# Kernel tuning notes

Measured on AMD Instinct MI355X. Metric: run time of the kernel, lower is better.

Reference implementation:

```python
import jax, jax.numpy as jnp
import numpy as np

WS = 8          # window size
SHIFT = WS // 2 # cyclic shift for shifted windows
HEADS = 6
C = 192
EMB = 256
HID = 4 * C
EPS = 1e-5


def _inorm(x):
    # InstanceNorm2d (affine=False): normalize each (sample, channel) over spatial dims
    m = x.mean(axis=(2, 3), keepdims=True)
    v = x.var(axis=(2, 3), keepdims=True)
    return (x - m) * jax.lax.rsqrt(v + EPS)


def _rel_index(ws):
    c = jnp.stack(jnp.meshgrid(jnp.arange(ws), jnp.arange(ws), indexing='ij'), -1).reshape(-1, 2)
    r = c[:, None] - c[None, :] + (ws - 1)          # (N,N,2) in [0, 2ws-2]
    return r[..., 0] * (2 * ws - 1) + r[..., 1]     # (N,N)


def _attn_mask(H, W, ws, shift):
    # standard Swin shifted-window mask: tokens from different pre-shift regions can't attend
    def ids(L):
        a = jnp.arange(L)
        return (a >= L - ws).astype(jnp.int32) + (a >= L - shift).astype(jnp.int32)
    img = ids(H)[:, None] * 3 + ids(W)[None, :]                     # (H,W)
    imgw = img.reshape(H // ws, ws, W // ws, ws).transpose(0, 2, 1, 3).reshape(-1, ws * ws)  # (nW,N)
    return jnp.where(imgw[:, None, :] != imgw[:, :, None], -1e9, 0.0)  # (nW,N,N)


def setup_inputs() -> dict:
    key = jax.random.key(0)
    ks = jax.random.split(key, 12)
    s = 0.02
    return {
        'x':        jax.random.normal(ks[0], (8, C, 128, 128), jnp.float32),
        'cond':     jax.random.normal(ks[1], (8, EMB), jnp.float32),
        'qkv_w':    jax.random.normal(ks[2], (3 * C, C), jnp.float32) * s,
        'qkv_b':    jnp.zeros((3 * C,), jnp.float32),
        'proj_w':   jax.random.normal(ks[3], (C, C), jnp.float32) * s,
        'proj_b':   jnp.zeros((C,), jnp.float32),
        'rel_bias': jax.random.normal(ks[4], ((2 * WS - 1) ** 2, HEADS), jnp.float32) * s,
        'film_w':   jax.random.normal(ks[5], (2 * C, EMB), jnp.float32) * s,
        'film_b':   jnp.zeros((2 * C,), jnp.float32),
        'mlp_w1':   jax.random.normal(ks[6], (HID, C), jnp.float32) * s,
        'mlp_b1':   jnp.zeros((HID,), jnp.float32),
        'mlp_w2':   jax.random.normal(ks[7], (C, HID), jnp.float32) * s,
        'mlp_b2':   jnp.zeros((C,), jnp.float32),
    }


def reference(x, cond, qkv_w, qkv_b, proj_w, proj_b, rel_bias,
              film_w, film_b, mlp_w1, mlp_b1, mlp_w2, mlp_b2):
    B, Cc, H, W = x.shape
    N = WS * WS
    nW = (H // WS) * (W // WS)
    hd = Cc // HEADS

    # ---- x = x + attn(norm1(x)) : shifted window attention ----
    xn = _inorm(x)
    xs = jnp.roll(xn, (-SHIFT, -SHIFT), axis=(2, 3))
    # window partition -> (B, nW, N, C)
    xw = (xs.reshape(B, Cc, H // WS, WS, W // WS, WS)
            .transpose(0, 2, 4, 3, 5, 1)
            .reshape(B, nW, N, Cc))
    qkv = xw @ qkv_w.T + qkv_b                       # (B,nW,N,3C)
    q, k, v = jnp.split(qkv, 3, axis=-1)
    def heads(t):
        return t.reshape(B, nW, N, HEADS, hd).transpose(0, 1, 3, 2, 4)  # (B,nW,H,N,hd)
    q, k, v = heads(q), heads(k), heads(v)
    attn = jnp.einsum('bwhnd,bwhmd->bwhnm', q, k) * (hd ** -0.5)
    bias = rel_bias[_rel_index(WS)].transpose(2, 0, 1)   # (HEADS,N,N)
    mask = _attn_mask(H, W, WS, SHIFT)                   # (nW,N,N)
    attn = attn + bias[None, None] + mask[None, :, None]
    a = jax.nn.softmax(attn, axis=-1)
    o = jnp.einsum('bwhnm,bwhmd->bwhnd', a, v)
    o = o.transpose(0, 1, 3, 2, 4).reshape(B, nW, N, Cc)
    o = o @ proj_w.T + proj_b
    # window reverse -> (B,C,H,W), undo shift
    o = (o.reshape(B, H // WS, W // WS, WS, WS, Cc)
           .transpose(0, 5, 1, 3, 2, 4)
           .reshape(B, Cc, H, W))
    o = jnp.roll(o, (SHIFT, SHIFT), axis=(2, 3))
    x = x + o

    # ---- x = x + mlp(FiLM(norm2(x), cond)) ----
    h = _inorm(x)
    gb = cond @ film_w.T + film_b                     # (B,2C)
    scale, shift = gb[:, :Cc], gb[:, Cc:]
    h = h * (1.0 + scale)[:, :, None, None] + shift[:, :, None, None]
    h = jnp.einsum('bchw,oc->bohw', h, mlp_w1) + mlp_b1[None, :, None, None]
    h = jax.nn.gelu(h, approximate=True)              # GELU('tanh')
    h = jnp.einsum('bchw,oc->bohw', h, mlp_w2) + mlp_b2[None, :, None, None]
    return x + h
```

## Files before the change

kernel.cpp:

```cpp
#include <hip/hip_runtime.h>
#include <hip/hip_bf16.h>

using bf16 = __hip_bfloat16;

#define HEADS 6
#define EPSV 1e-5f
#define QS 0.17677669529663687f

typedef __bf16 bfv8 __attribute__((ext_vector_type(8)));
typedef short sv8 __attribute__((ext_vector_type(8)));
typedef float fv4 __attribute__((ext_vector_type(4)));

__device__ __forceinline__ float bf2f(bf16 h) { return __bfloat162float(h); }

__device__ __forceinline__ unsigned short f2bfbits(float f) {
  union { float f; unsigned u; } x{f};
  unsigned r = x.u + 0x7fffu + ((x.u >> 16) & 1u);
  return (unsigned short)(r >> 16);
}

__device__ __forceinline__ int swz(int row, int col, int rowstride) {
  return row * rowstride + ((((col >> 3) ^ (row & 7)) << 3) | (col & 7));
}

__device__ __forceinline__ uint2 pack4b(fv4 a, float b0, float b1, float b2, float b3) {
  uint2 r;
  r.x = (unsigned)f2bfbits(a[0] + b0) | ((unsigned)f2bfbits(a[1] + b1) << 16);
  r.y = (unsigned)f2bfbits(a[2] + b2) | ((unsigned)f2bfbits(a[3] + b3) << 16);
  return r;
}

template <bool BW>
__device__ __forceinline__ bfv8 ldwf(const short* wb, const float* wf, int row,
                                     int k, int ld, float scale) {
  if constexpr (BW) {
    return *(const bfv8*)(wb + (size_t)row * ld + k);
  } else {
    const float* p = wf + (size_t)row * ld + k;
    float4 a = *(const float4*)p;
    float4 b = *(const float4*)(p + 4);
    sv8 s;
    s[0] = (short)f2bfbits(a.x * scale); s[1] = (short)f2bfbits(a.y * scale);
    s[2] = (short)f2bfbits(a.z * scale); s[3] = (short)f2bfbits(a.w * scale);
    s[4] = (short)f2bfbits(b.x * scale); s[5] = (short)f2bfbits(b.y * scale);
    s[6] = (short)f2bfbits(b.z * scale); s[7] = (short)f2bfbits(b.w * scale);
    return __builtin_bit_cast(bfv8, s);
  }
}

__global__ __launch_bounds__(256) void stats_kernel(const float* __restrict__ x,
                                                    float* __restrict__ mean,
                                                    float* __restrict__ rstd) {
  int bc = blockIdx.x;
  const float4* p = (const float4*)(x + (size_t)bc * 16384);
  float s = 0.f, s2 = 0.f;
  for (int i = threadIdx.x; i < 4096; i += 256) {
    float4 v = p[i];
    s += v.x + v.y + v.z + v.w;
    s2 = fmaf(v.x, v.x, s2);
    s2 = fmaf(v.y, v.y, s2);
    s2 = fmaf(v.z, v.z, s2);
    s2 = fmaf(v.w, v.w, s2);
  }
#pragma unroll
  for (int off = 32; off > 0; off >>= 1) {
    s += __shfl_down(s, off);
    s2 += __shfl_down(s2, off);
  }
  __shared__ float rs[4], rs2[4];
  int wid = threadIdx.x >> 6;
  if ((threadIdx.x & 63) == 0) { rs[wid] = s; rs2[wid] = s2; }
  __syncthreads();
  if (threadIdx.x == 0) {
    float S = rs[0] + rs[1] + rs[2] + rs[3];
    float S2 = rs2[0] + rs2[1] + rs2[2] + rs2[3];
    float m = S * (1.f / 16384.f);
    float v = S2 * (1.f / 16384.f) - m * m;
    mean[bc] = m;
    rstd[bc] = rsqrtf(v + EPSV);
  }
}

__device__ __forceinline__ void pack8(float4 a, float4 b, float sc, short* dst) {
  uint4 o;
  o.x = (unsigned)f2bfbits(a.x * sc) | ((unsigned)f2bfbits(a.y * sc) << 16);
  o.y = (unsigned)f2bfbits(a.z * sc) | ((unsigned)f2bfbits(a.w * sc) << 16);
  o.z = (unsigned)f2bfbits(b.x * sc) | ((unsigned)f2bfbits(b.y * sc) << 16);
  o.w = (unsigned)f2bfbits(b.z * sc) | ((unsigned)f2bfbits(b.w * sc) << 16);
  *(uint4*)dst = o;
}

__global__ __launch_bounds__(256) void fc_kernel(
    const float* __restrict__ cond, const float* __restrict__ fw,
    const float* __restrict__ fb, float* __restrict__ gb,
    const float* __restrict__ qkv_w, const float* __restrict__ proj_w,
    const float* __restrict__ mlp_w1, const float* __restrict__ mlp_w2,
    short* __restrict__ wbA, int nUnits) {
  int bid = blockIdx.x;
  if (bid < 12) {
    int g = bid * 256 + threadIdx.x;
    if (g >= 8 * 384) return;
    int b = g / 384, o = g % 384;
    const float* c = cond + b * 256;
    const float* w = fw + o * 256;
    float acc = fb[o];
    for (int k = 0; k < 256; k += 4) {
      float4 cv = *(const float4*)(c + k);
      float4 wv = *(const float4*)(w + k);
      acc = fmaf(cv.x, wv.x, acc);
      acc = fmaf(cv.y, wv.y, acc);
      acc = fmaf(cv.z, wv.z, acc);
      acc = fmaf(cv.w, wv.w, acc);
    }
    gb[g] = acc;
    return;
  }
  int u = (bid - 12) * 256 + threadIdx.x;
  if (u >= nUnits) return;
  if (u < 18432) {
    int e = u * 8;
    float sc = (e < 36864) ? QS : 1.f;
    const float* src = (e < 110592) ? (qkv_w + e) : (proj_w + (e - 110592));
    pack8(*(const float4*)src, *(const float4*)(src + 4), sc, wbA + e);
  } else if (u < 36864) {
    int f = (u - 18432) * 8;
    int ob = f / 12288, s = f % 12288;
    int row = s / 192, within = s % 192;
    int col0 = (((within >> 3) ^ (row & 7)) << 3);
    const float* src = mlp_w1 + (size_t)(ob * 64 + row) * 192 + col0;
    pack8(*(const float4*)src, *(const float4*)(src + 4), 1.f, wbA + 147456 + f);
  } else {
    int f = (u - 36864) * 8;
    int ob = f / 12288, s = f % 12288;
    int row = s / 64, within = s % 64;
    int ol = (((within >> 3) ^ (row & 7)) << 3);
    const float* src = mlp_w2 + (size_t)row * 768 + ob * 64 + ol;
    pack8(*(const float4*)src, *(const float4*)(src + 4), 1.f, wbA + 294912 + f);
  }
}

template <bool BW>
__global__ __launch_bounds__(512, 4) void attn_mfma2_kernel(
    const float* __restrict__ x, const float* __restrict__ mean,
    const float* __restrict__ rstd, const short* __restrict__ wb,
    const float* __restrict__ qkv_w, const float* __restrict__ qkv_b,
    const float* __restrict__ proj_w, const float* __restrict__ proj_b,
    const float* __restrict__ rel_bias, float* __restrict__ out) {
  __shared__ __align__(16) short s_x[64 * 192];
  __shared__ __align__(16) short s_k[64 * 192];
  __shared__ __align__(16) short s_v[192 * 64];
  __shared__ float s_rel[1350];

  const short* wbq = wb;
  const short* wbp = wb + 110592;

  int tid = threadIdx.x;
  int blk = ((blockIdx.x & 7) << 8) + (blockIdx.x >> 3);
  int b = blk >> 8;
  int wdw = blk & 255;
  int wh = wdw >> 4, ww = wdw & 15;
  int lane = tid & 63;
  int w = tid >> 6;
  int nloc = lane & 15, lg = lane >> 4;

  for (int i = tid; i < 1350; i += 512) s_rel[i] = rel_bias[i];

  for (int u = tid; u < 3072; u += 512) {
    int jh = u & 1, ii = (u >> 1) & 7, c = u >> 4;
    int hg = (wh * 8 + ii + 4) & 127;
    int wc0 = (ww * 8 + jh * 4 + 4) & 127;
    float4 v = *(const float4*)&x[((size_t)(b * 192 + c) << 14) + (hg << 7) + wc0];
    float mn = mean[b * 192 + c], rs = rstd[b * 192 + c];
    int n0 = ii * 8 + jh * 4;
    s_x[swz(n0 + 0, c, 192)] = (short)f2bfbits((v.x - mn) * rs);
    s_x[swz(n0 + 1, c, 192)] = (short)f2bfbits((v.y - mn) * rs);
    s_x[swz(n0 + 2, c, 192)] = (short)f2bfbits((v.z - mn) * rs);
    s_x[swz(n0 + 3, c, 192)] = (short)f2bfbits((v.w - mn) * rs);
  }
  __syncthreads();

  for (int half = 0; half < 2; half++) {
    int ptb = half * 2;
    bfv8 xf[2][6];
#pragma unroll
    for (int pp = 0; pp < 2; pp++)
#pragma unroll
      for (int ks = 0; ks < 6; ks++)
        xf[pp][ks] = *(const bfv8*)&s_x[swz((ptb + pp) * 16 + nloc, ks * 32 + lg * 8, 192)];
    __syncthreads();

    for (int t = w; t < 36; t += 8) {
      bool isQK = (t < 24);
      int baserow = isQK ? t * 16 : 384 + (t - 24) * 16;
      float scl = (!BW && t < 12) ? QS : 1.f;
      bfv8 wf[6];
#pragma unroll
      for (int ks = 0; ks < 6; ks++)
        wf[ks] = ldwf<BW>(wbq, qkv_w, baserow + nloc, ks * 32 + lg * 8, 192, scl);
#pragma unroll
      for (int pp = 0; pp < 2; pp++) {
        int pt = ptb + pp;
        fv4 acc = fv4{0.f, 0.f, 0.f, 0.f};
        if (isQK) {
#pragma unroll
          for (int ks = 0; ks < 6; ks++)
            acc = __builtin_amdgcn_mfma_f32_16x16x32_bf16(wf[ks], xf[pp][ks], acc, 0, 0, 0);
          int o0 = t * 16 + lg * 4;
          float4 bb = *(const float4*)&qkv_b[o0];
          float bsc = (t < 12) ? QS : 1.f;
          uint2 pkk = pack4b(acc, bb.x * bsc, bb.y * bsc, bb.z * bsc, bb.w * bsc);
          if (t < 12)
            *(uint2*)&s_x[swz(pt * 16 + nloc, o0, 192)] = pkk;
          else
            *(uint2*)&s_k[swz(pt * 16 + nloc, o0 - 192, 192)] = pkk;
        } else {
#pragma unroll
          for (int ks = 0; ks < 6; ks++)
            acc = __builtin_amdgcn_mfma_f32_16x16x32_bf16(xf[pp][ks], wf[ks], acc, 0, 0, 0);
          int d = (t - 24) * 16 + nloc;
          float bv = qkv_b[384 + d];
          *(uint2*)&s_v[swz(d, pt * 16 + lg * 4, 64)] = pack4b(acc, bv, bv, bv, bv);
        }
      }
    }
  }
  __syncthreads();

  int maskh = (wh == 15), maskw = (ww == 15);
#pragma unroll
  for (int ui = 0; ui < 3; ui++) {
    int u = w * 3 + ui;
    int hh = u >> 2, ng = u & 3;
    int n = ng * 16 + nloc;
    int i1 = n >> 3, j1 = n & 7;
    int gn = (maskh ? (i1 < 4 ? 1 : 2) : 0) * 3 + (maskw ? (j1 < 4 ? 1 : 2) : 0);

    bfv8 qf = *(const bfv8*)&s_x[swz(n, hh * 32 + lg * 8, 192)];
    fv4 sc[4];
#pragma unroll
    for (int mt = 0; mt < 4; mt++) {
      bfv8 kf = *(const bfv8*)&s_k[swz(mt * 16 + nloc, hh * 32 + lg * 8, 192)];
      sc[mt] = __builtin_amdgcn_mfma_f32_16x16x32_bf16(kf, qf, fv4{0.f, 0.f, 0.f, 0.f}, 0, 0, 0);
    }
    float vals[16];
#pragma unroll
    for (int mt = 0; mt < 4; mt++) {
#pragma unroll
      for (int r = 0; r < 4; r++) {
        int m = mt * 16 + lg * 4 + r;
        int i2 = m >> 3, j2 = m & 7;
        int gm = (maskh ? (i2 < 4 ? 1 : 2) : 0) * 3 + (maskw ? (j2 < 4 ? 1 : 2) : 0);
        float v = sc[mt][r] + s_rel[((i1 - i2 + 7) * 15 + (j1 - j2 + 7)) * 6 + hh];
        vals[mt * 4 + r] = (gn == gm) ? v : v - 1e9f;
      }
    }
    float mx = vals[0];
#pragma unroll
    for (int q = 1; q < 16; q++) mx = fmaxf(mx, vals[q]);
    mx = fmaxf(mx, __shfl_xor(mx, 16));
    mx = fmaxf(mx, __shfl_xor(mx, 32));
    float sum = 0.f;
#pragma unroll
    for (int q = 0; q < 16; q++) {
      vals[q] = __expf(vals[q] - mx);
      sum += vals[q];
    }
    sum += __shfl_xor(sum, 16);
    sum += __shfl_xor(sum, 32);
    float inv = 1.f / sum;

    unsigned pk[4][2];
#pragma unroll
    for (int mt = 0; mt < 4; mt++) {
      pk[mt][0] = (unsigned)f2bfbits(vals[mt * 4] * inv) |
                  ((unsigned)f2bfbits(vals[mt * 4 + 1] * inv) << 16);
      pk[mt][1] = (unsigned)f2bfbits(vals[mt * 4 + 2] * inv) |
                  ((unsigned)f2bfbits(vals[mt * 4 + 3] * inv) << 16);
    }
    int sel = lg >> 1;
    int S0 = nloc + ((lg & 1) << 5);
    int S1 = S0 + 16;
    bfv8 pf[2];
#pragma unroll
    for (int ks = 0; ks < 2; ks++) {
      unsigned a0 = (unsigned)__shfl((int)pk[2 * ks][0], S0);
      unsigned b0 = (unsigned)__shfl((int)pk[2 * ks + 1][0], S0);
      unsigned a1 = (unsigned)__shfl((int)pk[2 * ks][1], S0);
      unsigned b1 = (unsigned)__shfl((int)pk[2 * ks + 1][1], S0);
      unsigned a2 = (unsigned)__shfl((int)pk[2 * ks][0], S1);
      unsigned b2 = (unsigned)__shfl((int)pk[2 * ks + 1][0], S1);
      unsigned a3 = (unsigned)__shfl((int)pk[2 * ks][1], S1);
      unsigned b3 = (unsigned)__shfl((int)pk[2 * ks + 1][1], S1);
      uint4 uu;
      uu.x = sel ? b0 : a0;
      uu.y = sel ? b1 : a1;
      uu.z = sel ? b2 : a2;
      uu.w = sel ? b3 : a3;
      pf[ks] = __builtin_bit_cast(bfv8, uu);
    }
#pragma unroll
    for (int dt = 0; dt < 2; dt++) {
      fv4 oa = fv4{0.f, 0.f, 0.f, 0.f};
#pragma unroll
      for (int ks = 0; ks < 2; ks++) {
        bfv8 vf = *(const bfv8*)&s_v[swz(hh * 32 + dt * 16 + nloc, ks * 32 + lg * 8, 64)];
        oa = __builtin_amdgcn_mfma_f32_16x16x32_bf16(vf, pf[ks], oa, 0, 0, 0);
      }
      int d0 = hh * 32 + dt * 16 + lg * 4;
      *(uint2*)&s_x[swz(n, d0, 192)] = pack4b(oa, 0.f, 0.f, 0.f, 0.f);
    }
  }
  __syncthreads();

  {
    int a2 = w >> 1, half = w & 1;
#pragma unroll
    for (int ci = 0; ci < 3; ci++) {
      int ct = a2 * 3 + ci;
      bfv8 wf[6];
#pragma unroll
      for (int ks = 0; ks < 6; ks++)
        wf[ks] = ldwf<BW>(wbp, proj_w, ct * 16 + nloc, ks * 32 + lg * 8, 192, 1.f);
#pragma unroll
      for (int ni = 0; ni < 2; ni++) {
        int nt = half * 2 + ni;
        fv4 acc = fv4{0.f, 0.f, 0.f, 0.f};
#pragma unroll
        for (int ks = 0; ks < 6; ks++) {
          bfv8 of = *(const bfv8*)&s_x[swz(nt * 16 + nloc, ks * 32 + lg * 8, 192)];
          acc = __builtin_amdgcn_mfma_f32_16x16x32_bf16(wf[ks], of, acc, 0, 0, 0);
        }
        int n = nt * 16 + nloc;
        int ii = n >> 3, jj = n & 7;
        int hg = (wh * 8 + ii + 4) & 127;
        int wc = (ww * 8 + jj + 4) & 127;
        float4 pb4 = *(const float4*)&proj_b[ct * 16 + lg * 4];
        const float* pbp = &pb4.x;
#pragma unroll
        for (int r = 0; r < 4; r++) {
          int c = ct * 16 + lg * 4 + r;
          size_t gi = ((size_t)(b * 192 + c) << 14) + (hg << 7) + wc;
          out[gi] = x[gi] + acc[r] + pbp[r];
        }
      }
    }
  }
}

__global__ __launch_bounds__(512, 4) void mlp_mfma2_kernel(
    float* __restrict__ xio, const float* __restrict__ mean,
    const float* __restrict__ rstd, const float* __restrict__ gb,
    const short* __restrict__ w1s, const short* __restrict__ w2s,
    const float* __restrict__ b1, const float* __restrict__ b2) {
  __shared__ __align__(16) short s_pool[128 * 192];
  __shared__ __align__(16) short s_h[128 * 64];
  __shared__ float s_b1[768];
  __shared__ float s_mean[192], s_rstd[192], s_scale[192], s_shift[192], s_b2[192];

  int tid = threadIdx.x;
  int blk = blockIdx.x;
  int b = blk >> 7;
  int p0 = (blk & 127) << 7;
  int lane = tid & 63;
  int w = tid >> 6;

  for (int i = tid; i < 768; i += 512) s_b1[i] = b1[i];
  for (int i = tid; i < 192; i += 512) {
    int bc = b * 192 + i;
    s_mean[i] = mean[bc];
    s_rstd[i] = rstd[bc];
    s_scale[i] = 1.f + gb[b * 384 + i];
    s_shift[i] = gb[b * 384 + 192 + i];
    s_b2[i] = b2[i];
  }
  __syncthreads();

  for (int e = tid; e < 3072; e += 512) {
    int p = e & 127, cb = e >> 7;
    int c0 = cb * 8;
    sv8 pk;
#pragma unroll
    for (int j = 0; j < 8; j++) {
      int c = c0 + j;
      float xv = xio[((size_t)(b * 192 + c) << 14) + p0 + p];
      float hn = (xv - s_mean[c]) * s_rstd[c];
      pk[j] = (short)f2bfbits(hn * s_scale[c] + s_shift[c]);
    }
    *(sv8*)&s_pool[swz(p, c0, 192)] = pk;
  }
  __syncthreads();

  int prow = w * 16 + (lane & 15);
  bfv8 afr[6];
#pragma unroll
  for (int ks = 0; ks < 6; ks++) {
    int c = ks * 32 + (lane >> 4) * 8;
    afr[ks] = *(const bfv8*)&s_pool[swz(prow, c, 192)];
  }

  short* s_w1 = s_pool;
  short* s_w2 = s_pool + 12288;
  char* poolBytes = (char*)s_pool;

  fv4 acc2[12];
#pragma unroll
  for (int i = 0; i < 12; i++) acc2[i] = fv4{0.f, 0.f, 0.f, 0.f};

  for (int ob = 0; ob < 12; ob++) {
    __syncthreads();
    const char* g1 = (const char*)(w1s + ob * 12288);
    const char* g2 = (const char*)(w2s + ob * 12288);
#pragma unroll
    for (int i = 0; i < 3; i++) {
      int ch = w * 3 + i;
      __builtin_amdgcn_global_load_lds(
          (const __attribute__((address_space(1))) void*)(g1 + ch * 1024 + lane * 16),
          (__attribute__((address_space(3))) void*)(poolBytes + ch * 1024), 16, 0, 0);
      __builtin_amdgcn_global_load_lds(
          (const __attribute__((address_space(1))) void*)(g2 + ch * 1024 + lane * 16),
          (__attribute__((address_space(3))) void*)(poolBytes + 24576 + ch * 1024), 16, 0, 0);
    }
    __syncthreads();

#pragma unroll
    for (int it = 0; it < 4; it++) {
      fv4 a1 = fv4{0.f, 0.f, 0.f, 0.f};
      int orow = it * 16 + (lane & 15);
#pragma unroll
      for (int ks = 0; ks < 6; ks++) {
        int c = ks * 32 + (lane >> 4) * 8;
        bfv8 wf = *(const bfv8*)&s_w1[swz(orow, c, 192)];
        a1 = __builtin_amdgcn_mfma_f32_16x16x32_bf16(wf, afr[ks], a1, 0, 0, 0);
      }
      int o0 = ob * 64 + it * 16 + (lane >> 4) * 4;
      unsigned short hb[4];
#pragma unroll
      for (int r = 0; r < 4; r++) {
        float v = a1[r] + s_b1[o0 + r];
        float g = v / (1.f + __expf(-1.5957691216f * fmaf(0.044715f * v * v, v, v)));
        hb[r] = f2bfbits(g);
      }
      uint2 pk;
      pk.x = (unsigned)hb[0] | ((unsigned)hb[1] << 16);
      pk.y = (unsigned)hb[2] | ((unsigned)hb[3] << 16);
      int ol = it * 16 + (lane >> 4) * 4;
      *(uint2*)&s_h[swz(prow, ol, 64)] = pk;
    }

#pragma unroll
    for (int ks2 = 0; ks2 < 2; ks2++) {
      int ol = ks2 * 32 + (lane >> 4) * 8;
      bfv8 hf = *(const bfv8*)&s_h[swz(prow, ol, 64)];
#pragma unroll
      for (int it2 = 0; it2 < 12; it2++) {
        int crow = it2 * 16 + (lane & 15);
        bfv8 w2f = *(const bfv8*)&s_w2[swz(crow, ol, 64)];
        acc2[it2] = __builtin_amdgcn_mfma_f32_16x16x32_bf16(w2f, hf, acc2[it2], 0, 0, 0);
      }
    }
  }

  int p = p0 + w * 16 + (lane & 15);
#pragma unroll
  for (int it2 = 0; it2 < 12; it2++) {
    int c0 = it2 * 16 + (lane >> 4) * 4;
#pragma unroll
    for (int r = 0; r < 4; r++) {
      int c = c0 + r;
      size_t gi = ((size_t)(b * 192 + c) << 14) + p;
      xio[gi] += acc2[it2][r] + s_b2[c];
    }
  }
}

__global__ __launch_bounds__(512, 2) void mlp_mfma_kernel(
    float* __restrict__ xio, const float* __restrict__ mean,
    const float* __restrict__ rstd, const float* __restrict__ gb,
    const float* __restrict__ w1, const float* __restrict__ b1,
    const float* __restrict__ w2, const float* __restrict__ b2) {
  __shared__ __align__(16) short s_a[128 * 192];
  __shared__ __align__(16) short s_h[128 * 64];
  __shared__ __align__(16) short s_w1[64 * 192];
  __shared__ __align__(16) short s_w2[192 * 64];
  __shared__ float s_b1[768];
  __shared__ float s_mean[192], s_rstd[192], s_scale[192], s_shift[192], s_b2[192];

  int tid = threadIdx.x;
  int blk = blockIdx.x;
  int b = blk >> 7;
  int p0 = (blk & 127) << 7;
  int lane = tid & 63;
  int w = tid >> 6;

  for (int i = tid; i < 768; i += 512) s_b1[i] = b1[i];
  for (int i = tid; i < 192; i += 512) {
    int bc = b * 192 + i;
    s_mean[i] = mean[bc];
    s_rstd[i] = rstd[bc];
    s_scale[i] = 1.f + gb[b * 384 + i];
    s_shift[i] = gb[b * 384 + 192 + i];
    s_b2[i] = b2[i];
  }
  __syncthreads();

  for (int e = tid; e < 3072; e += 512) {
    int p = e & 127, cb = e >> 7;
    int c0 = cb * 8;
    sv8 pk;
#pragma unroll
    for (int j = 0; j < 8; j++) {
      int c = c0 + j;
      float xv = xio[((size_t)(b * 192 + c) << 14) + p0 + p];
      float hn = (xv - s_mean[c]) * s_rstd[c];
      pk[j] = (short)f2bfbits(hn * s_scale[c] + s_shift[c]);
    }
    *(sv8*)&s_a[swz(p, c0, 192)] = pk;
  }
  __syncthreads();

  int prow = w * 16 + (lane & 15);
  bfv8 afr[6];
#pragma unroll
  for (int ks = 0; ks < 6; ks++) {
    int c = ks * 32 + (lane >> 4) * 8;
    afr[ks] = *(const bfv8*)&s_a[swz(prow, c, 192)];
  }

  fv4 acc2[12];
#pragma unroll
  for (int i = 0; i < 12; i++) acc2[i] = fv4{0.f, 0.f, 0.f, 0.f};

  for (int ob = 0; ob < 12; ob++) {
    __syncthreads();
    for (int e = tid; e < 3072; e += 512) {
      int row = e / 48, ch4 = e % 48;
      float4 v = *(const float4*)&w1[(size_t)(ob * 64 + row) * 192 + ch4 * 4];
      uint2 pk;
      pk.x = (unsigned)f2bfbits(v.x) | ((unsigned)f2bfbits(v.y) << 16);
      pk.y = (unsigned)f2bfbits(v.z) | ((unsigned)f2bfbits(v.w) << 16);
      *(uint2*)&s_w1[swz(row, ch4 * 4, 192)] = pk;
    }
    for (int e = tid; e < 3072; e += 512) {
      int row = e >> 4, o4 = (e & 15) * 4;
      float4 v = *(const float4*)&w2[(size_t)row * 768 + ob * 64 + o4];
      uint2 pk;
      pk.x = (unsigned)f2bfbits(v.x) | ((unsigned)f2bfbits(v.y) << 16);
      pk.y = (unsigned)f2bfbits(v.z) | ((unsigned)f2bfbits(v.w) << 16);
      *(uint2*)&s_w2[swz(row, o4, 64)] = pk;
    }
    __syncthreads();

#pragma unroll
    for (int it = 0; it < 4; it++) {
      fv4 a1 = fv4{0.f, 0.f, 0.f, 0.f};
      int orow = it * 16 + (lane & 15);
#pragma unroll
      for (int ks = 0; ks < 6; ks++) {
        int c = ks * 32 + (lane >> 4) * 8;
        bfv8 wf = *(const bfv8*)&s_w1[swz(orow, c, 192)];
        a1 = __builtin_amdgcn_mfma_f32_16x16x32_bf16(wf, afr[ks], a1, 0, 0, 0);
      }
      int o0 = ob * 64 + it * 16 + (lane >> 4) * 4;
      unsigned short hb[4];
#pragma unroll
      for (int r = 0; r < 4; r++) {
        float v = a1[r] + s_b1[o0 + r];
        float g = v / (1.f + __expf(-1.5957691216f * fmaf(0.044715f * v * v, v, v)));
        hb[r] = f2bfbits(g);
      }
      uint2 pk;
      pk.x = (unsigned)hb[0] | ((unsigned)hb[1] << 16);
      pk.y = (unsigned)hb[2] | ((unsigned)hb[3] << 16);
      int ol = it * 16 + (lane >> 4) * 4;
      *(uint2*)&s_h[swz(prow, ol, 64)] = pk;
    }

#pragma unroll
    for (int ks2 = 0; ks2 < 2; ks2++) {
      int ol = ks2 * 32 + (lane >> 4) * 8;
      bfv8 hf = *(const bfv8*)&s_h[swz(prow, ol, 64)];
#pragma unroll
      for (int it2 = 0; it2 < 12; it2++) {
        int crow = it2 * 16 + (lane & 15);
        bfv8 w2f = *(const bfv8*)&s_w2[swz(crow, ol, 64)];
        acc2[it2] = __builtin_amdgcn_mfma_f32_16x16x32_bf16(w2f, hf, acc2[it2], 0, 0, 0);
      }
    }
  }

  int p = p0 + w * 16 + (lane & 15);
#pragma unroll
  for (int it2 = 0; it2 < 12; it2++) {
    int c0 = it2 * 16 + (lane >> 4) * 4;
#pragma unroll
    for (int r = 0; r < 4; r++) {
      int c = c0 + r;
      size_t gi = ((size_t)(b * 192 + c) << 14) + p;
      xio[gi] += acc2[it2][r] + s_b2[c];
    }
  }
}

extern "C" void kernel_launch(void* const* d_in, const int* in_sizes, int n_in,
                              void* d_out, int out_size, void* d_ws, size_t ws_size,
                              hipStream_t stream) {
  const float* x = (const float*)d_in[0];
  const float* cond = (const float*)d_in[1];
  const float* qkv_w = (const float*)d_in[2];
  const float* qkv_b = (const float*)d_in[3];
  const float* proj_w = (const float*)d_in[4];
  const float* proj_b = (const float*)d_in[5];
  const float* rel_bias = (const float*)d_in[6];
  const float* film_w = (const float*)d_in[7];
  const float* film_b = (const float*)d_in[8];
  const float* mlp_w1 = (const float*)d_in[9];
  const float* mlp_b1 = (const float*)d_in[10];
  const float* mlp_w2 = (const float*)d_in[11];
  const float* mlp_b2 = (const float*)d_in[12];

  float* out = (float*)d_out;
  float* ws = (float*)d_ws;
  float* mean1 = ws;
  float* rstd1 = ws + 1536;
  float* mean2 = ws + 3072;
  float* rstd2 = ws + 4608;
  float* gb = ws + 6144;
  short* wbA = (short*)(ws + 9216);

  bool haveA = ws_size >= (size_t)(36864 + 294912);
  bool haveM = ws_size >= (size_t)(36864 + 3 * 294912);

  int nUnits = haveM ? 55296 : (haveA ? 18432 : 0);
  fc_kernel<<<12 + (nUnits + 255) / 256, 256, 0, stream>>>(
      cond, film_w, film_b, gb, qkv_w, proj_w, mlp_w1, mlp_w2, wbA, nUnits);
  stats_kernel<<<1536, 256, 0, stream>>>(x, mean1, rstd1);

  if (haveA)
    attn_mfma2_kernel<true><<<2048, 512, 0, stream>>>(
        x, mean1, rstd1, wbA, qkv_w, qkv_b, proj_w, proj_b, rel_bias, out);
  else
    attn_mfma2_kernel<false><<<2048, 512, 0, stream>>>(
        x, mean1, rstd1, wbA, qkv_w, qkv_b, proj_w, proj_b, rel_bias, out);

  stats_kernel<<<1536, 256, 0, stream>>>(out, mean2, rstd2);

  if (haveM)
    mlp_mfma2_kernel<<<1024, 512, 0, stream>>>(out, mean2, rstd2, gb,
                                               wbA + 147456, wbA + 294912,
                                               mlp_b1, mlp_b2);
  else
    mlp_mfma_kernel<<<1024, 512, 0, stream>>>(out, mean2, rstd2, gb, mlp_w1,
                                              mlp_b1, mlp_w2, mlp_b2);
}
```

Baseline: 396.4 us.

## Fuse second norm stats into attention epilogue and merge pre-kernels

Computes per-channel partial sums and sums of squares of the attention output inside the attention kernel's projection epilogue, writes them per window block, and reduces them with a small kernel. This replaces the second full read of the output just to compute instance-norm statistics. It also folds the first stats pass into the weight-packing kernel to save a launch, software-pipelines weight loads in the QKV and projection loops, hoists the Q/K/V fragment loads, prefetches residual x values, and vectorises the MLP input staging with float4 loads. The cost is extra registers and workspace, and E[x^2]-m^2 computed from partials may differ slightly in precision.

```diff
diff --git a/kernel.cpp b/kernel.cpp
--- a/kernel.cpp
+++ b/kernel.cpp
@@ -10,8 +10,6 @@
 typedef __bf16 bfv8 __attribute__((ext_vector_type(8)));
 typedef short sv8 __attribute__((ext_vector_type(8)));
 typedef float fv4 __attribute__((ext_vector_type(4)));
-
-__device__ __forceinline__ float bf2f(bf16 h) { return __bfloat162float(h); }
 
 __device__ __forceinline__ unsigned short f2bfbits(float f) {
   union { float f; unsigned u; } x{f};
@@ -48,13 +46,11 @@
   }
 }
 
-__global__ __launch_bounds__(256) void stats_kernel(const float* __restrict__ x,
-                                                    float* __restrict__ mean,
-                                                    float* __restrict__ rstd) {
-  int bc = blockIdx.x;
+__device__ __forceinline__ void stats_body(const float* __restrict__ x, int bc,
+                                           float2* __restrict__ mr, int tid) {
   const float4* p = (const float4*)(x + (size_t)bc * 16384);
   float s = 0.f, s2 = 0.f;
-  for (int i = threadIdx.x; i < 4096; i += 256) {
+  for (int i = tid; i < 4096; i += 256) {
     float4 v = p[i];
     s += v.x + v.y + v.z + v.w;
     s2 = fmaf(v.x, v.x, s2);
@@ -68,17 +64,21 @@
     s2 += __shfl_down(s2, off);
   }
   __shared__ float rs[4], rs2[4];
-  int wid = threadIdx.x >> 6;
-  if ((threadIdx.x & 63) == 0) { rs[wid] = s; rs2[wid] = s2; }
+  int wid = tid >> 6;
+  if ((tid & 63) == 0) { rs[wid] = s; rs2[wid] = s2; }
   __syncthreads();
-  if (threadIdx.x == 0) {
+  if (tid == 0) {
     float S = rs[0] + rs[1] + rs[2] + rs[3];
     float S2 = rs2[0] + rs2[1] + rs2[2] + rs2[3];
     float m = S * (1.f / 16384.f);
     float v = S2 * (1.f / 16384.f) - m * m;
-    mean[bc] = m;
-    rstd[bc] = rsqrtf(v + EPSV);
-  }
+    mr[bc] = make_float2(m, rsqrtf(v + EPSV));
+  }
+}
+
+__global__ __launch_bounds__(256) void stats_kernel(const float* __restrict__ x,
+                                                    float2* __restrict__ mr) {
+  stats_body(x, blockIdx.x, mr, threadIdx.x);
 }
 
 __device__ __forceinline__ void pack8(float4 a, float4 b, float sc, short* dst) {
@@ -90,13 +90,19 @@
   *(uint4*)dst = o;
 }
 
-__global__ __launch_bounds__(256) void fc_kernel(
+__global__ __launch_bounds__(256) void fused_pre_kernel(
+    const float* __restrict__ x, float2* __restrict__ mr1,
     const float* __restrict__ cond, const float* __restrict__ fw,
     const float* __restrict__ fb, float* __restrict__ gb,
     const float* __restrict__ qkv_w, const float* __restrict__ proj_w,
     const float* __restrict__ mlp_w1, const float* __restrict__ mlp_w2,
     short* __restrict__ wbA, int nUnits) {
   int bid = blockIdx.x;
+  if (bid < 1536) {
+    stats_body(x, bid, mr1, threadIdx.x);
+    return;
+  }
+  bid -= 1536;
   if (bid < 12) {
     int g = bid * 256 + threadIdx.x;
     if (g >= 8 * 384) return;
@@ -139,13 +145,36 @@
   }
 }
 
+__global__ __launch_bounds__(64) void reduce2_kernel(const float2* __restrict__ part,
+                                                     float2* __restrict__ mr2) {
+  int bc = blockIdx.x;
+  int b = bc / 192, c = bc % 192;
+  const float2* p = part + (size_t)(b * 256) * 192 + c;
+  float s = 0.f, q = 0.f;
+  for (int k = threadIdx.x; k < 256; k += 64) {
+    float2 v = p[(size_t)k * 192];
+    s += v.x;
+    q += v.y;
+  }
+#pragma unroll
+  for (int off = 32; off > 0; off >>= 1) {
+    s += __shfl_down(s, off);
+    q += __shfl_down(q, off);
+  }
+  if (threadIdx.x == 0) {
+    float m = s * (1.f / 16384.f);
+    float v = q * (1.f / 16384.f) - m * m;
+    mr2[bc] = make_float2(m, rsqrtf(v + EPSV));
+  }
+}
+
 template <bool BW>
-__global__ __launch_bounds__(512, 4) void attn_mfma2_kernel(
-    const float* __restrict__ x, const float* __restrict__ mean,
-    const float* __restrict__ rstd, const short* __restrict__ wb,
-    const float* __restrict__ qkv_w, const float* __restrict__ qkv_b,
-    const float* __restrict__ proj_w, const float* __restrict__ proj_b,
-    const float* __restrict__ rel_bias, float* __restrict__ out) {
+__global__ __launch_bounds__(512, 4) void attn_mfma3_kernel(
+    const float* __restrict__ x, const float2* __restrict__ mr1,
+    const short* __restrict__ wb, const float* __restrict__ qkv_w,
+    const float* __restrict__ qkv_b, const float* __restrict__ proj_w,
+    const float* __restrict__ proj_b, const float* __restrict__ rel_bias,
+    float* __restrict__ out, float2* __restrict__ part) {
   __shared__ __align__(16) short s_x[64 * 192];
   __shared__ __align__(16) short s_k[64 * 192];
   __shared__ __align__(16) short s_v[192 * 64];
@@ -170,12 +199,12 @@
     int hg = (wh * 8 + ii + 4) & 127;
     int wc0 = (ww * 8 + jh * 4 + 4) & 127;
     float4 v = *(const float4*)&x[((size_t)(b * 192 + c) << 14) + (hg << 7) + wc0];
-    float mn = mean[b * 192 + c], rs = rstd[b * 192 + c];
+    float2 mrv = mr1[b * 192 + c];
     int n0 = ii * 8 + jh * 4;
-    s_x[swz(n0 + 0, c, 192)] = (short)f2bfbits((v.x - mn) * rs);
-    s_x[swz(n0 + 1, c, 192)] = (short)f2bfbits((v.y - mn) * rs);
-    s_x[swz(n0 + 2, c, 192)] = (short)f2bfbits((v.z - mn) * rs);
-    s_x[swz(n0 + 3, c, 192)] = (short)f2bfbits((v.w - mn) * rs);
+    s_x[swz(n0 + 0, c, 192)] = (short)f2bfbits((v.x - mrv.x) * mrv.y);
+    s_x[swz(n0 + 1, c, 192)] = (short)f2bfbits((v.y - mrv.x) * mrv.y);
+    s_x[swz(n0 + 2, c, 192)] = (short)f2bfbits((v.z - mrv.x) * mrv.y);
+    s_x[swz(n0 + 3, c, 192)] = (short)f2bfbits((v.w - mrv.x) * mrv.y);
   }
   __syncthreads();
 
@@ -189,14 +218,26 @@
         xf[pp][ks] = *(const bfv8*)&s_x[swz((ptb + pp) * 16 + nloc, ks * 32 + lg * 8, 192)];
     __syncthreads();
 
-    for (int t = w; t < 36; t += 8) {
+    bfv8 wf[6];
+    {
+      int t0 = w;
+      int baserow0 = (t0 < 24) ? t0 * 16 : 384 + (t0 - 24) * 16;
+      float scl0 = (!BW && t0 < 12) ? QS : 1.f;
+#pragma unroll
+      for (int ks = 0; ks < 6; ks++)
+        wf[ks] = ldwf<BW>(wbq, qkv_w, baserow0 + nloc, ks * 32 + lg * 8, 192, scl0);
+    }
+    for (int t = w; t < 36;) {
+      int tn = t + 8;
+      bfv8 wfn[6];
+      if (tn < 36) {
+        int baserown = (tn < 24) ? tn * 16 : 384 + (tn - 24) * 16;
+        float scln = (!BW && tn < 12) ? QS : 1.f;
+#pragma unroll
+        for (int ks = 0; ks < 6; ks++)
+          wfn[ks] = ldwf<BW>(wbq, qkv_w, baserown + nloc, ks * 32 + lg * 8, 192, scln);
+      }
       bool isQK = (t < 24);
-      int baserow = isQK ? t * 16 : 384 + (t - 24) * 16;
-      float scl = (!BW && t < 12) ? QS : 1.f;
-      bfv8 wf[6];
-#pragma unroll
-      for (int ks = 0; ks < 6; ks++)
-        wf[ks] = ldwf<BW>(wbq, qkv_w, baserow + nloc, ks * 32 + lg * 8, 192, scl);
 #pragma unroll
       for (int pp = 0; pp < 2; pp++) {
         int pt = ptb + pp;
@@ -222,11 +263,27 @@
           *(uint2*)&s_v[swz(d, pt * 16 + lg * 4, 64)] = pack4b(acc, bv, bv, bv, bv);
         }
       }
+      if (tn >= 36) break;
+#pragma unroll
+      for (int ks = 0; ks < 6; ks++) wf[ks] = wfn[ks];
+      t = tn;
     }
   }
   __syncthreads();
 
   int maskh = (wh == 15), maskw = (ww == 15);
+  bfv8 qfh[3];
+  bfv8 kfh[3][4];
+#pragma unroll
+  for (int ui = 0; ui < 3; ui++) {
+    int u = w * 3 + ui;
+    int hh = u >> 2, ng = u & 3;
+    int n = ng * 16 + nloc;
+    qfh[ui] = *(const bfv8*)&s_x[swz(n, hh * 32 + lg * 8, 192)];
+#pragma unroll
+    for (int mt = 0; mt < 4; mt++)
+      kfh[ui][mt] = *(const bfv8*)&s_k[swz(mt * 16 + nloc, hh * 32 + lg * 8, 192)];
+  }
 #pragma unroll
   for (int ui = 0; ui < 3; ui++) {
     int u = w * 3 + ui;
@@ -235,13 +292,18 @@
     int i1 = n >> 3, j1 = n & 7;
     int gn = (maskh ? (i1 < 4 ? 1 : 2) : 0) * 3 + (maskw ? (j1 < 4 ? 1 : 2) : 0);
 
-    bfv8 qf = *(const bfv8*)&s_x[swz(n, hh * 32 + lg * 8, 192)];
     fv4 sc[4];
 #pragma unroll
-    for (int mt = 0; mt < 4; mt++) {
-      bfv8 kf = *(const bfv8*)&s_k[swz(mt * 16 + nloc, hh * 32 + lg * 8, 192)];
-      sc[mt] = __builtin_amdgcn_mfma_f32_16x16x32_bf16(kf, qf, fv4{0.f, 0.f, 0.f, 0.f}, 0, 0, 0);
-    }
+    for (int mt = 0; mt < 4; mt++)
+      sc[mt] = __builtin_amdgcn_mfma_f32_16x16x32_bf16(kfh[ui][mt], qfh[ui],
+                                                       fv4{0.f, 0.f, 0.f, 0.f}, 0, 0, 0);
+    bfv8 vfh[2][2];
+#pragma unroll
+    for (int dt = 0; dt < 2; dt++)
+#pragma unroll
+      for (int ks = 0; ks < 2; ks++)
+        vfh[dt][ks] = *(const bfv8*)&s_v[swz(hh * 32 + dt * 16 + nloc, ks * 32 + lg * 8, 64)];
+
     float vals[16];
 #pragma unroll
     for (int mt = 0; mt < 4; mt++) {
@@ -302,10 +364,8 @@
     for (int dt = 0; dt < 2; dt++) {
       fv4 oa = fv4{0.f, 0.f, 0.f, 0.f};
 #pragma unroll
-      for (int ks = 0; ks < 2; ks++) {
-        bfv8 vf = *(const bfv8*)&s_v[swz(hh * 32 + dt * 16 + nloc, ks * 32 + lg * 8, 64)];
-        oa = __builtin_amdgcn_mfma_f32_16x16x32_bf16(vf, pf[ks], oa, 0, 0, 0);
-      }
+      for (int ks = 0; ks < 2; ks++)
+        oa = __builtin_amdgcn_mfma_f32_16x16x32_bf16(vfh[dt][ks], pf[ks], oa, 0, 0, 0);
       int d0 = hh * 32 + dt * 16 + lg * 4;
       *(uint2*)&s_x[swz(n, d0, 192)] = pack4b(oa, 0.f, 0.f, 0.f, 0.f);
     }
@@ -314,13 +374,49 @@
 
   {
     int a2 = w >> 1, half = w & 1;
+    int hgv[2], wcv[2];
+#pragma unroll
+    for (int ni = 0; ni < 2; ni++) {
+      int n = (half * 2 + ni) * 16 + nloc;
+      hgv[ni] = (wh * 8 + (n >> 3) + 4) & 127;
+      wcv[ni] = (ww * 8 + (n & 7) + 4) & 127;
+    }
+    float xres[3][2][4];
 #pragma unroll
     for (int ci = 0; ci < 3; ci++) {
       int ct = a2 * 3 + ci;
-      bfv8 wf[6];
-#pragma unroll
-      for (int ks = 0; ks < 6; ks++)
-        wf[ks] = ldwf<BW>(wbp, proj_w, ct * 16 + nloc, ks * 32 + lg * 8, 192, 1.f);
+#pragma unroll
+      for (int ni = 0; ni < 2; ni++)
+#pragma unroll
+        for (int r = 0; r < 4; r++) {
+          int c = ct * 16 + lg * 4 + r;
+          xres[ci][ni][r] =
+              x[((size_t)(b * 192 + c) << 14) + (hgv[ni] << 7) + wcv[ni]];
+        }
+    }
+
+    float ssum[3][4], ssq[3][4];
+#pragma unroll
+    for (int ci = 0; ci < 3; ci++)
+#pragma unroll
+      for (int r = 0; r < 4; r++) { ssum[ci][r] = 0.f; ssq[ci][r] = 0.f; }
+
+    bfv8 wfp[6];
+#pragma unroll
+    for (int ks = 0; ks < 6; ks++)
+      wfp[ks] = ldwf<BW>(wbp, proj_w, (a2 * 3) * 16 + nloc, ks * 32 + lg * 8, 192, 1.f);
+
+#pragma unroll
+    for (int ci = 0; ci < 3; ci++) {
+      int ct = a2 * 3 + ci;
+      bfv8 wfn[6];
+      if (ci < 2) {
+#pragma unroll
+        for (int ks = 0; ks < 6; ks++)
+          wfn[ks] = ldwf<BW>(wbp, proj_w, (ct + 1) * 16 + nloc, ks * 32 + lg * 8, 192, 1.f);
+      }
+      float4 pb4 = *(const float4*)&proj_b[ct * 16 + lg * 4];
+      const float* pbp = &pb4.x;
 #pragma unroll
       for (int ni = 0; ni < 2; ni++) {
         int nt = half * 2 + ni;
@@ -328,30 +424,60 @@
 #pragma unroll
         for (int ks = 0; ks < 6; ks++) {
           bfv8 of = *(const bfv8*)&s_x[swz(nt * 16 + nloc, ks * 32 + lg * 8, 192)];
-          acc = __builtin_amdgcn_mfma_f32_16x16x32_bf16(wf[ks], of, acc, 0, 0, 0);
+          acc = __builtin_amdgcn_mfma_f32_16x16x32_bf16(wfp[ks], of, acc, 0, 0, 0);
         }
-        int n = nt * 16 + nloc;
-        int ii = n >> 3, jj = n & 7;
-        int hg = (wh * 8 + ii + 4) & 127;
-        int wc = (ww * 8 + jj + 4) & 127;
-        float4 pb4 = *(const float4*)&proj_b[ct * 16 + lg * 4];
-        const float* pbp = &pb4.x;
 #pragma unroll
         for (int r = 0; r < 4; r++) {
           int c = ct * 16 + lg * 4 + r;
-          size_t gi = ((size_t)(b * 192 + c) << 14) + (hg << 7) + wc;
-          out[gi] = x[gi] + acc[r] + pbp[r];
+          size_t gi = ((size_t)(b * 192 + c) << 14) + (hgv[ni] << 7) + wcv[ni];
+          float v = xres[ci][ni][r] + acc[r] + pbp[r];
+          out[gi] = v;
+          ssum[ci][r] += v;
+          ssq[ci][r] = fmaf(v, v, ssq[ci][r]);
         }
       }
-    }
-  }
-}
-
-__global__ __launch_bounds__(512, 4) void mlp_mfma2_kernel(
-    float* __restrict__ xio, const float* __restrict__ mean,
-    const float* __restrict__ rstd, const float* __restrict__ gb,
-    const short* __restrict__ w1s, const short* __restrict__ w2s,
-    const float* __restrict__ b1, const float* __restrict__ b2) {
+      if (ci < 2) {
+#pragma unroll
+        for (int ks = 0; ks < 6; ks++) wfp[ks] = wfn[ks];
+      }
+    }
+
+    if (part) {
+      float* redS = (float*)s_rel;
+      float* redQ = redS + 384;
+#pragma unroll
+      for (int ci = 0; ci < 3; ci++) {
+        int ct = a2 * 3 + ci;
+#pragma unroll
+        for (int r = 0; r < 4; r++) {
+          float s = ssum[ci][r], q = ssq[ci][r];
+#pragma unroll
+          for (int m = 1; m < 16; m <<= 1) {
+            s += __shfl_xor(s, m);
+            q += __shfl_xor(q, m);
+          }
+          if (nloc == 0) {
+            int c = ct * 16 + lg * 4 + r;
+            redS[c * 2 + half] = s;
+            redQ[c * 2 + half] = q;
+          }
+        }
+      }
+      __syncthreads();
+      if (tid < 192) {
+        float s = redS[tid * 2] + redS[tid * 2 + 1];
+        float q = redQ[tid * 2] + redQ[tid * 2 + 1];
+        part[(size_t)blk * 192 + tid] = make_float2(s, q);
+      }
+    }
+  }
+}
+
+__global__ __launch_bounds__(512, 4) void mlp_mfma3_kernel(
+    float* __restrict__ xio, const float2* __restrict__ mr2,
+    const float* __restrict__ gb, const short* __restrict__ w1s,
+    const short* __restrict__ w2s, const float* __restrict__ b1,
+    const float* __restrict__ b2) {
   __shared__ __align__(16) short s_pool[128 * 192];
   __shared__ __align__(16) short s_h[128 * 64];
   __shared__ float s_b1[768];
@@ -366,27 +492,40 @@
 
   for (int i = tid; i < 768; i += 512) s_b1[i] = b1[i];
   for (int i = tid; i < 192; i += 512) {
-    int bc = b * 192 + i;
-    s_mean[i] = mean[bc];
-    s_rstd[i] = rstd[bc];
+    float2 mrv = mr2[b * 192 + i];
+    s_mean[i] = mrv.x;
+    s_rstd[i] = mrv.y;
     s_scale[i] = 1.f + gb[b * 384 + i];
     s_shift[i] = gb[b * 384 + 192 + i];
     s_b2[i] = b2[i];
   }
   __syncthreads();
 
-  for (int e = tid; e < 3072; e += 512) {
-    int p = e & 127, cb = e >> 7;
-    int c0 = cb * 8;
-    sv8 pk;
+  for (int e = tid; e < 768; e += 512) {
+    int pq = e & 31, cb = e >> 5;
+    int p = pq * 4, c0 = cb * 8;
+    float4 xv[8];
+#pragma unroll
+    for (int j = 0; j < 8; j++)
+      xv[j] = *(const float4*)&xio[((size_t)(b * 192 + c0 + j) << 14) + p0 + p];
 #pragma unroll
     for (int j = 0; j < 8; j++) {
       int c = c0 + j;
-      float xv = xio[((size_t)(b * 192 + c) << 14) + p0 + p];
-      float hn = (xv - s_mean[c]) * s_rstd[c];
-      pk[j] = (short)f2bfbits(hn * s_scale[c] + s_shift[c]);
-    }
-    *(sv8*)&s_pool[swz(p, c0, 192)] = pk;
+      float mn = s_mean[c], rs = s_rstd[c], scv = s_scale[c], sh = s_shift[c];
+      xv[j].x = (xv[j].x - mn) * rs * scv + sh;
+      xv[j].y = (xv[j].y - mn) * rs * scv + sh;
+      xv[j].z = (xv[j].z - mn) * rs * scv + sh;
+      xv[j].w = (xv[j].w - mn) * rs * scv + sh;
+    }
+#pragma unroll
+    for (int pp = 0; pp < 4; pp++) {
+      sv8 pk;
+      const float* base = &xv[0].x;
+#pragma unroll
+      for (int j = 0; j < 8; j++) pk[j] = (short)f2bfbits((&xv[j].x)[pp]);
+      (void)base;
+      *(sv8*)&s_pool[swz(p + pp, c0, 192)] = pk;
+    }
   }
   __syncthreads();
 
@@ -474,10 +613,10 @@
 }
 
 __global__ __launch_bounds__(512, 2) void mlp_mfma_kernel(
-    float* __restrict__ xio, const float* __restrict__ mean,
-    const float* __restrict__ rstd, const float* __restrict__ gb,
-    const float* __restrict__ w1, const float* __restrict__ b1,
-    const float* __restrict__ w2, const float* __restrict__ b2) {
+    float* __restrict__ xio, const float2* __restrict__ mr2,
+    const float* __restrict__ gb, const float* __restrict__ w1,
+    const float* __restrict__ b1, const float* __restrict__ w2,
+    const float* __restrict__ b2) {
   __shared__ __align__(16) short s_a[128 * 192];
   __shared__ __align__(16) short s_h[128 * 64];
   __shared__ __align__(16) short s_w1[64 * 192];
@@ -494,9 +633,9 @@
 
   for (int i = tid; i < 768; i += 512) s_b1[i] = b1[i];
   for (int i = tid; i < 192; i += 512) {
-    int bc = b * 192 + i;
-    s_mean[i] = mean[bc];
-    s_rstd[i] = rstd[bc];
+    float2 mrv = mr2[b * 192 + i];
+    s_mean[i] = mrv.x;
+    s_rstd[i] = mrv.y;
     s_scale[i] = 1.f + gb[b * 384 + i];
     s_shift[i] = gb[b * 384 + 192 + i];
     s_b2[i] = b2[i];
@@ -619,36 +758,42 @@
   const float* mlp_b2 = (const float*)d_in[12];
 
   float* out = (float*)d_out;
-  float* ws = (float*)d_ws;
-  float* mean1 = ws;
-  float* rstd1 = ws + 1536;
-  float* mean2 = ws + 3072;
-  float* rstd2 = ws + 4608;
-  float* gb = ws + 6144;
-  short* wbA = (short*)(ws + 9216);
-
-  bool haveA = ws_size >= (size_t)(36864 + 294912);
-  bool haveM = ws_size >= (size_t)(36864 + 3 * 294912);
+  char* wsb = (char*)d_ws;
+
+  float2* mr1 = (float2*)wsb;
+  float2* mr2 = (float2*)(wsb + 12288);
+  float* gb = (float*)(wsb + 24576);
+  const size_t base = 36864;
+  const size_t partB = 2048ull * 192 * 8;
+  const size_t wbB = 442368ull * 2;
+
+  bool fuseP = ws_size >= base + partB + wbB;
+  bool haveM = fuseP || ws_size >= base + wbB;
+  bool haveA = ws_size >= base + 294912;
+
+  float2* part = fuseP ? (float2*)(wsb + base) : nullptr;
+  short* wbA = (short*)(wsb + base + (fuseP ? partB : 0));
 
   int nUnits = haveM ? 55296 : (haveA ? 18432 : 0);
-  fc_kernel<<<12 + (nUnits + 255) / 256, 256, 0, stream>>>(
-      cond, film_w, film_b, gb, qkv_w, proj_w, mlp_w1, mlp_w2, wbA, nUnits);
-  stats_kernel<<<1536, 256, 0, stream>>>(x, mean1, rstd1);
+  fused_pre_kernel<<<1536 + 12 + (nUnits + 255) / 256, 256, 0, stream>>>(
+      x, mr1, cond, film_w, film_b, gb, qkv_w, proj_w, mlp_w1, mlp_w2, wbA, nUnits);
 
   if (haveA)
-    attn_mfma2_kernel<true><<<2048, 512, 0, stream>>>(
-        x, mean1, rstd1, wbA, qkv_w, qkv_b, proj_w, proj_b, rel_bias, out);
+    attn_mfma3_kernel<true><<<2048, 512, 0, stream>>>(
+        x, mr1, wbA, qkv_w, qkv_b, proj_w, proj_b, rel_bias, out, part);
   else
-    attn_mfma2_kernel<false><<<2048, 512, 0, stream>>>(
-        x, mean1, rstd1, wbA, qkv_w, qkv_b, proj_w, proj_b, rel_bias, out);
-
-  stats_kernel<<<1536, 256, 0, stream>>>(out, mean2, rstd2);
+    attn_mfma3_kernel<false><<<2048, 512, 0, stream>>>(
+        x, mr1, wbA, qkv_w, qkv_b, proj_w, proj_b, rel_bias, out, part);
+
+  if (part)
+    reduce2_kernel<<<1536, 64, 0, stream>>>(part, mr2);
+  else
+    stats_kernel<<<1536, 256, 0, stream>>>(out, mr2);
 
   if (haveM)
-    mlp_mfma2_kernel<<<1024, 512, 0, stream>>>(out, mean2, rstd2, gb,
-                                               wbA + 147456, wbA + 294912,
-                                               mlp_b1, mlp_b2);
+    mlp_mfma3_kernel<<<1024, 512, 0, stream>>>(out, mr2, gb, wbA + 147456,
+                                               wbA + 294912, mlp_b1, mlp_b2);
   else
-    mlp_mfma_kernel<<<1024, 512, 0, stream>>>(out, mean2, rstd2, gb, mlp_w1,
-                                              mlp_b1, mlp_w2, mlp_b2);
-}
+    mlp_mfma_kernel<<<1024, 512, 0, stream>>>(out, mr2, gb, mlp_w1, mlp_b1,
+                                              mlp_w2, mlp_b2);
+}
```

Result: slower. 526.9 us (+32.9%).
